# Kernel optimization log

Hardware: AMD Instinct MI355X
Metric: run time of the kernel (lower is better)

## Reference

```python
import jax, jax.numpy as jnp
import numpy as np
import math

D_MODEL = 1024
N_HEADS = 16
D_K = D_MODEL // N_HEADS
B, S = 4, 2048


def setup_inputs() -> dict:
    key = jax.random.key(0)
    ks = jax.random.split(key, 11)
    std = 1.0 / math.sqrt(D_MODEL)
    inp = {
        "query": jax.random.normal(ks[0], (B, S, D_MODEL), dtype=jnp.float32),
        "key_in": jax.random.normal(ks[1], (B, S, D_MODEL), dtype=jnp.float32),
        "value": jax.random.normal(ks[2], (B, S, D_MODEL), dtype=jnp.float32),
        "Wq": jax.random.normal(ks[3], (D_MODEL, D_MODEL), dtype=jnp.float32) * std,
        "bq": jnp.zeros((D_MODEL,), dtype=jnp.float32),
        "Wk": jax.random.normal(ks[4], (D_MODEL, D_MODEL), dtype=jnp.float32) * std,
        "bk": jnp.zeros((D_MODEL,), dtype=jnp.float32),
        "Wv": jax.random.normal(ks[5], (D_MODEL, D_MODEL), dtype=jnp.float32) * std,
        "bv": jnp.zeros((D_MODEL,), dtype=jnp.float32),
        "Wo": jax.random.normal(ks[6], (D_MODEL, D_MODEL), dtype=jnp.float32) * std,
        "bo": jnp.zeros((D_MODEL,), dtype=jnp.float32),
    }
    return inp


def reference(query, key_in, value, Wq, bq, Wk, bk, Wv, bv, Wo, bo):
    b, s, _ = query.shape
    scale = math.sqrt(D_K)
    # projections: nn.Linear computes x @ W.T + b
    Q = (query @ Wq.T + bq).reshape(b, s, N_HEADS, D_K).transpose(0, 2, 1, 3)
    K = (key_in @ Wk.T + bk).reshape(b, s, N_HEADS, D_K).transpose(0, 2, 1, 3)
    V = (value @ Wv.T + bv).reshape(b, s, N_HEADS, D_K).transpose(0, 2, 1, 3)
    # [b, h, s, s]
    scores = jnp.einsum("bhqd,bhkd->bhqk", Q, K) / scale
    causal = jnp.tril(jnp.ones((s, s), dtype=bool))
    scores = jnp.where(causal[None, None, :, :], scores, jnp.float32(-1e9))
    attn = jax.nn.softmax(scores, axis=-1)
    out = jnp.einsum("bhqk,bhkd->bhqd", attn, V)
    out = out.transpose(0, 2, 1, 3).reshape(b, s, D_MODEL)
    return out @ Wo.T + bo
```

## Files before the change

kernel.cpp:

```cpp
#include <hip/hip_runtime.h>
#include <hip/hip_bf16.h>
#include <cstdint>

#define DM   1024
#define NH   16
#define DKK  64
#define BB   4
#define SS   2048

typedef __attribute__((ext_vector_type(8)))  short short8;
typedef __attribute__((ext_vector_type(4)))  float f32x4;
typedef __attribute__((ext_vector_type(16))) float f32x16;

__device__ __forceinline__ unsigned short f2bf(float f) {
    union { float f; uint32_t u; } v; v.f = f;
    uint32_t u = v.u;
    uint32_t r = (u + 0x7FFFu + ((u >> 16) & 1u)) >> 16;
    return (unsigned short)r;
}

__global__ void cvt_all(const float4* __restrict__ q, const float4* __restrict__ k,
                        const float4* __restrict__ v, const float4* __restrict__ wq,
                        const float4* __restrict__ wk, const float4* __restrict__ wv,
                        const float4* __restrict__ wo, ushort4* __restrict__ dst)
{
    const int NA = 2097152, NW = 262144;
    int i = blockIdx.x * 256 + threadIdx.x;
    const float4* s;
    if (i < 3 * NA) {
        int a = i >> 21, off = i & (NA - 1);
        s = (a == 0 ? q : a == 1 ? k : v) + off;
    } else {
        int j = i - 3 * NA;
        int a = j >> 18, off = j & (NW - 1);
        s = (a == 0 ? wq : a == 1 ? wk : a == 2 ? wv : wo) + off;
    }
    float4 f = *s;
    ushort4 o;
    o.x = f2bf(f.x); o.y = f2bf(f.y); o.z = f2bf(f.z); o.w = f2bf(f.w);
    dst[i] = o;
}

__global__ void gemm_qkv(const unsigned short* __restrict__ Aq,
                         const unsigned short* __restrict__ Ak,
                         const unsigned short* __restrict__ Av,
                         const unsigned short* __restrict__ Wq,
                         const unsigned short* __restrict__ Wk,
                         const unsigned short* __restrict__ Wv,
                         const float* __restrict__ bq,
                         const float* __restrict__ bk,
                         const float* __restrict__ bv,
                         unsigned short* __restrict__ Qo,
                         unsigned short* __restrict__ Ko,
                         unsigned short* __restrict__ Vo,
                         const float qscale)
{
    const int z = blockIdx.z;
    const unsigned short* A  = (z == 0) ? Aq : (z == 1) ? Ak : Av;
    const unsigned short* Bw = (z == 0) ? Wq : (z == 1) ? Wk : Wv;
    const float* bias        = (z == 0) ? bq : (z == 1) ? bk : bv;

    __shared__ unsigned short lA[128 * 64];
    __shared__ unsigned short lB[128 * 64];
    const int tid = threadIdx.x;
    const int w = tid >> 6, l = tid & 63;
    const int brow = blockIdx.y * 128;
    const int bcol = blockIdx.x * 128;
    const int wr = (w >> 1) * 64, wc = (w & 1) * 64;
    const int lrow = l & 15;
    const int lk = (l >> 4) * 8;
    const int sr = l >> 3;
    const int sc = (l & 7) * 8;
    f32x4 acc[4][4] = {};

    for (int k0 = 0; k0 < 1024; k0 += 64) {
#pragma unroll
        for (int i = 0; i < 4; ++i) {
            const int chunk = w * 4 + i;
            const int r = chunk * 8 + sr;
            const unsigned short* ga = A  + (size_t)(brow + r) * 1024 + k0 + sc;
            const unsigned short* gb = Bw + (size_t)(bcol + r) * 1024 + k0 + sc;
            __builtin_amdgcn_global_load_lds((__attribute__((address_space(1))) void*)ga,
                                             (__attribute__((address_space(3))) void*)(lA + chunk * 512),
                                             16, 0, 0);
            __builtin_amdgcn_global_load_lds((__attribute__((address_space(1))) void*)gb,
                                             (__attribute__((address_space(3))) void*)(lB + chunk * 512),
                                             16, 0, 0);
        }
        asm volatile("s_waitcnt vmcnt(0)" ::: "memory");
        __syncthreads();
#pragma unroll
        for (int kk = 0; kk < 2; ++kk) {
            short8 af[4], bfr[4];
#pragma unroll
            for (int m = 0; m < 4; ++m)
                af[m] = *(const short8*)(lA + (wr + m * 16 + lrow) * 64 + kk * 32 + lk);
#pragma unroll
            for (int n = 0; n < 4; ++n)
                bfr[n] = *(const short8*)(lB + (wc + n * 16 + lrow) * 64 + kk * 32 + lk);
#pragma unroll
            for (int m = 0; m < 4; ++m)
#pragma unroll
                for (int n = 0; n < 4; ++n)
                    acc[m][n] = __builtin_amdgcn_mfma_f32_16x16x32_bf16(af[m], bfr[n], acc[m][n], 0, 0, 0);
        }
        __syncthreads();
    }

    const float ascale = (z == 0) ? qscale : 1.0f;
#pragma unroll
    for (int m = 0; m < 4; ++m) {
#pragma unroll
        for (int n = 0; n < 4; ++n) {
            const int i0 = brow + wr + m * 16 + (l >> 4) * 4;
            const int j  = bcol + wc + n * 16 + lrow;
            const float bj = bias[j];
            const int hh = j >> 6, d = j & 63;
            if (z < 2) {
                unsigned short* Cb = (z == 0) ? Qo : Ko;
#pragma unroll
                for (int t = 0; t < 4; ++t) {
                    const int i = i0 + t;
                    const int b = i >> 11, s = i & 2047;
                    Cb[(((size_t)(b * NH + hh) * SS) + s) * DKK + d] = f2bf((acc[m][n][t] + bj) * ascale);
                }
            } else {
                const int b = i0 >> 11, s0 = i0 & 2047;
                ushort4 pk;
                pk.x = f2bf(acc[m][n][0] + bj);
                pk.y = f2bf(acc[m][n][1] + bj);
                pk.z = f2bf(acc[m][n][2] + bj);
                pk.w = f2bf(acc[m][n][3] + bj);
                *(ushort4*)(Vo + (((size_t)(b * NH + hh) * DKK) + d) * SS + s0) = pk;
            }
        }
    }
}

__global__ void gemm_out(const unsigned short* __restrict__ A,
                         const unsigned short* __restrict__ Bw,
                         const float* __restrict__ bias,
                         float* __restrict__ Cout)
{
    __shared__ unsigned short lA[128 * 64];
    __shared__ unsigned short lB[128 * 64];
    const int tid = threadIdx.x;
    const int w = tid >> 6, l = tid & 63;
    const int brow = blockIdx.y * 128;
    const int bcol = blockIdx.x * 128;
    const int wr = (w >> 1) * 64, wc = (w & 1) * 64;
    const int lrow = l & 15;
    const int lk = (l >> 4) * 8;
    const int sr = l >> 3;
    const int sc = (l & 7) * 8;
    f32x4 acc[4][4] = {};

    for (int k0 = 0; k0 < 1024; k0 += 64) {
#pragma unroll
        for (int i = 0; i < 4; ++i) {
            const int chunk = w * 4 + i;
            const int r = chunk * 8 + sr;
            const unsigned short* ga = A  + (size_t)(brow + r) * 1024 + k0 + sc;
            const unsigned short* gb = Bw + (size_t)(bcol + r) * 1024 + k0 + sc;
            __builtin_amdgcn_global_load_lds((__attribute__((address_space(1))) void*)ga,
                                             (__attribute__((address_space(3))) void*)(lA + chunk * 512),
                                             16, 0, 0);
            __builtin_amdgcn_global_load_lds((__attribute__((address_space(1))) void*)gb,
                                             (__attribute__((address_space(3))) void*)(lB + chunk * 512),
                                             16, 0, 0);
        }
        asm volatile("s_waitcnt vmcnt(0)" ::: "memory");
        __syncthreads();
#pragma unroll
        for (int kk = 0; kk < 2; ++kk) {
            short8 af[4], bfr[4];
#pragma unroll
            for (int m = 0; m < 4; ++m)
                af[m] = *(const short8*)(lA + (wr + m * 16 + lrow) * 64 + kk * 32 + lk);
#pragma unroll
            for (int n = 0; n < 4; ++n)
                bfr[n] = *(const short8*)(lB + (wc + n * 16 + lrow) * 64 + kk * 32 + lk);
#pragma unroll
            for (int m = 0; m < 4; ++m)
#pragma unroll
                for (int n = 0; n < 4; ++n)
                    acc[m][n] = __builtin_amdgcn_mfma_f32_16x16x32_bf16(af[m], bfr[n], acc[m][n], 0, 0, 0);
        }
        __syncthreads();
    }

#pragma unroll
    for (int m = 0; m < 4; ++m) {
#pragma unroll
        for (int n = 0; n < 4; ++n) {
            const int i0 = brow + wr + m * 16 + (l >> 4) * 4;
            const int j  = bcol + wc + n * 16 + lrow;
            const float bj = bias[j];
#pragma unroll
            for (int t = 0; t < 4; ++t)
                Cout[(size_t)(i0 + t) * DM + j] = acc[m][n][t] + bj;
        }
    }
}

__global__ __launch_bounds__(256) void attn_kernel(
        const unsigned short* __restrict__ Q,
        const unsigned short* __restrict__ K,
        const unsigned short* __restrict__ Vt,
        unsigned short* __restrict__ AO)
{
    const int flat = blockIdx.y * 16 + blockIdx.x;
    const int r8 = flat & 7, k8 = flat >> 3;
    const int bh = r8 * 8 + (k8 & 7);
    const int qchunk = 15 - (k8 >> 3);
    const int tid = threadIdx.x;
    const int w = tid >> 6, l = tid & 63;
    const int ln = l & 31, h = l >> 5;
    const int qb = qchunk * 128;
    const int q0w = qb + w * 32;

    __shared__ __align__(16) char lK[2][4096];
    __shared__ __align__(16) char lV[2][4096];

    const unsigned short* Qp = Q  + ((size_t)bh * SS + q0w) * DKK;
    const unsigned short* Kp = K  + (size_t)bh * SS * DKK;
    const unsigned short* Vp = Vt + (size_t)bh * DKK * SS;

    const int srow = tid >> 3, scb = tid & 7;
    const int swb = srow * 128 + ((scb * 16) ^ ((srow & 7) << 4));
    const unsigned short* ksrc = Kp + srow * DKK + scb * 8;
    const int vd = (scb < 4) ? srow : (srow + 32);
    const unsigned short* vsrc = Vp + (size_t)vd * SS + (scb & 3) * 8;

    int ka[4], va[4];
#pragma unroll
    for (int ks = 0; ks < 4; ++ks)
        ka[ks] = ln * 128 + ((ks * 32 + h * 16) ^ ((ln & 7) << 4));
#pragma unroll
    for (int c = 0; c < 4; ++c)
        va[c] = ln * 128 + ((c * 32 + h * 16) ^ ((ln & 7) << 4));

    short8 qf[4];
#pragma unroll
    for (int ks = 0; ks < 4; ++ks)
        qf[ks] = *(const short8*)(Qp + (size_t)ln * DKK + ks * 16 + h * 8);

    f32x16 o0 = {}, o1 = {};
    float lsum = 0.f;

    const int Tc = qb / 32;
    const int NT = Tc + 4;

    auto compute = [&](int t, int buf) {
        const char* kb = lK[buf];
        const char* vb = lV[buf];
        short8 kf[4];
#pragma unroll
        for (int ks = 0; ks < 4; ++ks) kf[ks] = *(const short8*)(kb + ka[ks]);

        f32x16 s = {};
        __builtin_amdgcn_s_setprio(1);
#pragma unroll
        for (int ks = 0; ks < 4; ++ks)
            s = __builtin_amdgcn_mfma_f32_32x32x16_bf16(kf[ks], qf[ks], s, 0, 0, 0);
        __builtin_amdgcn_s_setprio(0);

        const bool diag = (t == Tc + w);
#pragma unroll
        for (int r = 0; r < 16; ++r) {
            float e;
            asm("v_exp_f32 %0, %1" : "=v"(e) : "v"(s[r]));
            if (diag) {
                const int crow = (r & 3) + 8 * (r >> 2) + 4 * h;
                e = (crow > ln) ? 0.f : e;
            }
            s[r] = e;
            lsum += e;
        }

        uint32_t pk[8];
#pragma unroll
        for (int i = 0; i < 8; ++i) {
            uint32_t d;
            asm("v_cvt_pk_bf16_f32 %0, %1, %2" : "=v"(d) : "v"(s[2 * i]), "v"(s[2 * i + 1]));
            pk[i] = d;
        }
        asm("v_permlane32_swap_b32 %0, %1" : "+v"(pk[0]), "+v"(pk[2]));
        asm("v_permlane32_swap_b32 %0, %1" : "+v"(pk[1]), "+v"(pk[3]));
        asm("v_permlane32_swap_b32 %0, %1" : "+v"(pk[4]), "+v"(pk[6]));
        asm("v_permlane32_swap_b32 %0, %1" : "+v"(pk[5]), "+v"(pk[7]));

        union Ux { uint32_t u[4]; short8 s8; } pa0, pa1;
        pa0.u[0] = pk[0]; pa0.u[1] = pk[1]; pa0.u[2] = pk[2]; pa0.u[3] = pk[3];
        pa1.u[0] = pk[4]; pa1.u[1] = pk[5]; pa1.u[2] = pk[6]; pa1.u[3] = pk[7];

        short8 vf00 = *(const short8*)(vb + va[0]);
        short8 vf10 = *(const short8*)(vb + va[1]);
        short8 vf01 = *(const short8*)(vb + va[2]);
        short8 vf11 = *(const short8*)(vb + va[3]);

        __builtin_amdgcn_s_setprio(1);
        o0 = __builtin_amdgcn_mfma_f32_32x32x16_bf16(pa0.s8, vf00, o0, 0, 0, 0);
        o0 = __builtin_amdgcn_mfma_f32_32x32x16_bf16(pa1.s8, vf10, o0, 0, 0, 0);
        o1 = __builtin_amdgcn_mfma_f32_32x32x16_bf16(pa0.s8, vf01, o1, 0, 0, 0);
        o1 = __builtin_amdgcn_mfma_f32_32x32x16_bf16(pa1.s8, vf11, o1, 0, 0, 0);
        __builtin_amdgcn_s_setprio(0);
    };

    short8 kA = *(const short8*)(ksrc);
    short8 vA = *(const short8*)(vsrc);
    *(short8*)(&lK[0][swb]) = kA;
    *(short8*)(&lV[0][swb]) = vA;
    kA = *(const short8*)(ksrc + 2048);
    vA = *(const short8*)(vsrc + 32);
    short8 kB = {}, vB = {};
    __syncthreads();

    int t = 0, buf = 0;
    for (;;) {
        if (t + 2 < NT) {
            kB = *(const short8*)(ksrc + (size_t)(t + 2) * 2048);
            vB = *(const short8*)(vsrc + (size_t)(t + 2) * 32);
        }
        if (t <= Tc + w) compute(t, buf);
        if (t + 1 < NT) {
            *(short8*)(&lK[buf ^ 1][swb]) = kA;
            *(short8*)(&lV[buf ^ 1][swb]) = vA;
        }
        __syncthreads();
        buf ^= 1;
        if (++t == NT) break;

        if (t + 2 < NT) {
            kA = *(const short8*)(ksrc + (size_t)(t + 2) * 2048);
            vA = *(const short8*)(vsrc + (size_t)(t + 2) * 32);
        }
        if (t <= Tc + w) compute(t, buf);
        if (t + 1 < NT) {
            *(short8*)(&lK[buf ^ 1][swb]) = kB;
            *(short8*)(&lV[buf ^ 1][swb]) = vB;
        }
        __syncthreads();
        buf ^= 1;
        if (++t == NT) break;
    }

    lsum += __shfl_xor(lsum, 32, 64);
    const float rcp = 1.0f / lsum;

    const int bb = bh >> 4, hh = bh & 15;
#pragma unroll
    for (int r = 0; r < 16; ++r) {
        const int crow = (r & 3) + 8 * (r >> 2) + 4 * h;
        const float rl = __shfl(rcp, crow, 64);
        const size_t row = (size_t)(bb * SS + q0w + crow) * DM + hh * DKK;
        AO[row + ln]      = f2bf(o0[r] * rl);
        AO[row + 32 + ln] = f2bf(o1[r] * rl);
    }
}

extern "C" void kernel_launch(void* const* d_in, const int* in_sizes, int n_in,
                              void* d_out, int out_size, void* d_ws, size_t ws_size,
                              hipStream_t stream)
{
    const float* query  = (const float*)d_in[0];
    const float* key_in = (const float*)d_in[1];
    const float* value  = (const float*)d_in[2];
    const float* Wq = (const float*)d_in[3];
    const float* bq = (const float*)d_in[4];
    const float* Wk = (const float*)d_in[5];
    const float* bk = (const float*)d_in[6];
    const float* Wv = (const float*)d_in[7];
    const float* bv = (const float*)d_in[8];
    const float* Wo = (const float*)d_in[9];
    const float* bo = (const float*)d_in[10];

    const size_t NACT = (size_t)BB * SS * DM;
    const size_t NWT  = (size_t)DM * DM;

    unsigned short* ws  = (unsigned short*)d_ws;
    unsigned short* qin = ws;
    unsigned short* kin = qin + NACT;
    unsigned short* vin = kin + NACT;
    unsigned short* wqb = vin + NACT;
    unsigned short* wkb = wqb + NWT;
    unsigned short* wvb = wkb + NWT;
    unsigned short* wob = wvb + NWT;
    unsigned short* Qb  = wob + NWT;
    unsigned short* Kb  = Qb + NACT;
    unsigned short* Vtb = Kb + NACT;
    unsigned short* AOb = Vtb + NACT;

    const int n4 = (int)(3 * (NACT / 4) + 4 * (NWT / 4));
    cvt_all<<<n4 / 256, 256, 0, stream>>>((const float4*)query, (const float4*)key_in,
                                          (const float4*)value, (const float4*)Wq,
                                          (const float4*)Wk, (const float4*)Wv,
                                          (const float4*)Wo, (ushort4*)ws);

    const float QSCALE = 0.125f * 1.44269504088896f;
    dim3 gq(DM / 128, (BB * SS) / 128, 3);
    gemm_qkv<<<gq, 256, 0, stream>>>(qin, kin, vin, wqb, wkb, wvb,
                                     bq, bk, bv, Qb, Kb, Vtb, QSCALE);

    attn_kernel<<<dim3(16, 64), 256, 0, stream>>>(Qb, Kb, Vtb, AOb);

    dim3 gg(DM / 128, (BB * SS) / 128);
    gemm_out<<<gg, 256, 0, stream>>>(AOb, wob, bo, (float*)d_out);
}
```

Baseline: 190.3 us.

## Fuse activation fp32->bf16 conversion into QKV GEMM and remap block order

Removes the separate conversion pass over the three fp32 activation tensors. The QKV GEMM now loads fp32 directly, converts to bf16 in registers with v_cvt_pk_bf16_f32, and writes the result to LDS, so the bf16 copies are never written out and read back. Only the weights are still pre-converted. Both GEMMs also remap block IDs so that consecutive blocks spread across the 8 column tiles, which is meant to improve L2 or per-die cache locality. The cost is that the A-tile loads become synchronous register loads instead of async global_load_lds, and they read twice as many bytes per tile.

Measured after the change: 175.2 us. -7.9%, faster.

```diff
diff --git a/kernel.cpp b/kernel.cpp
--- a/kernel.cpp
+++ b/kernel.cpp
@@ -19,31 +19,23 @@
     return (unsigned short)r;
 }
 
-__global__ void cvt_all(const float4* __restrict__ q, const float4* __restrict__ k,
-                        const float4* __restrict__ v, const float4* __restrict__ wq,
-                        const float4* __restrict__ wk, const float4* __restrict__ wv,
-                        const float4* __restrict__ wo, ushort4* __restrict__ dst)
+__global__ void cvt_w(const float4* __restrict__ wq, const float4* __restrict__ wk,
+                      const float4* __restrict__ wv, const float4* __restrict__ wo,
+                      ushort4* __restrict__ dst)
 {
-    const int NA = 2097152, NW = 262144;
+    const int NW = 262144;
     int i = blockIdx.x * 256 + threadIdx.x;
-    const float4* s;
-    if (i < 3 * NA) {
-        int a = i >> 21, off = i & (NA - 1);
-        s = (a == 0 ? q : a == 1 ? k : v) + off;
-    } else {
-        int j = i - 3 * NA;
-        int a = j >> 18, off = j & (NW - 1);
-        s = (a == 0 ? wq : a == 1 ? wk : a == 2 ? wv : wo) + off;
-    }
+    int a = i >> 18, off = i & (NW - 1);
+    const float4* s = (a == 0 ? wq : a == 1 ? wk : a == 2 ? wv : wo) + off;
     float4 f = *s;
     ushort4 o;
     o.x = f2bf(f.x); o.y = f2bf(f.y); o.z = f2bf(f.z); o.w = f2bf(f.w);
     dst[i] = o;
 }
 
-__global__ void gemm_qkv(const unsigned short* __restrict__ Aq,
-                         const unsigned short* __restrict__ Ak,
-                         const unsigned short* __restrict__ Av,
+__global__ void gemm_qkv(const float* __restrict__ Aq,
+                         const float* __restrict__ Ak,
+                         const float* __restrict__ Av,
                          const unsigned short* __restrict__ Wq,
                          const unsigned short* __restrict__ Wk,
                          const unsigned short* __restrict__ Wv,
@@ -55,8 +47,14 @@
                          unsigned short* __restrict__ Vo,
                          const float qscale)
 {
-    const int z = blockIdx.z;
-    const unsigned short* A  = (z == 0) ? Aq : (z == 1) ? Ak : Av;
+    const int orig = blockIdx.z * 512 + blockIdx.y * 8 + blockIdx.x;
+    const int wid  = (orig & 7) * 192 + (orig >> 3);
+    const int z    = wid >> 9;
+    const int rem  = wid & 511;
+    const int brow = (rem >> 3) * 128;
+    const int bcol = (rem & 7) * 128;
+
+    const float* A           = (z == 0) ? Aq : (z == 1) ? Ak : Av;
     const unsigned short* Bw = (z == 0) ? Wq : (z == 1) ? Wk : Wv;
     const float* bias        = (z == 0) ? bq : (z == 1) ? bk : bv;
 
@@ -64,8 +62,6 @@
     __shared__ unsigned short lB[128 * 64];
     const int tid = threadIdx.x;
     const int w = tid >> 6, l = tid & 63;
-    const int brow = blockIdx.y * 128;
-    const int bcol = blockIdx.x * 128;
     const int wr = (w >> 1) * 64, wc = (w & 1) * 64;
     const int lrow = l & 15;
     const int lk = (l >> 4) * 8;
@@ -78,14 +74,24 @@
         for (int i = 0; i < 4; ++i) {
             const int chunk = w * 4 + i;
             const int r = chunk * 8 + sr;
-            const unsigned short* ga = A  + (size_t)(brow + r) * 1024 + k0 + sc;
             const unsigned short* gb = Bw + (size_t)(bcol + r) * 1024 + k0 + sc;
-            __builtin_amdgcn_global_load_lds((__attribute__((address_space(1))) void*)ga,
-                                             (__attribute__((address_space(3))) void*)(lA + chunk * 512),
-                                             16, 0, 0);
             __builtin_amdgcn_global_load_lds((__attribute__((address_space(1))) void*)gb,
                                              (__attribute__((address_space(3))) void*)(lB + chunk * 512),
                                              16, 0, 0);
+        }
+#pragma unroll
+        for (int i = 0; i < 4; ++i) {
+            const int chunk = w * 4 + i;
+            const int r = chunk * 8 + sr;
+            const float* ga = A + (size_t)(brow + r) * 1024 + k0 + sc;
+            float4 f0 = *(const float4*)(ga);
+            float4 f1 = *(const float4*)(ga + 4);
+            union { uint32_t u[4]; short8 s8; } c;
+            asm("v_cvt_pk_bf16_f32 %0, %1, %2" : "=v"(c.u[0]) : "v"(f0.x), "v"(f0.y));
+            asm("v_cvt_pk_bf16_f32 %0, %1, %2" : "=v"(c.u[1]) : "v"(f0.z), "v"(f0.w));
+            asm("v_cvt_pk_bf16_f32 %0, %1, %2" : "=v"(c.u[2]) : "v"(f1.x), "v"(f1.y));
+            asm("v_cvt_pk_bf16_f32 %0, %1, %2" : "=v"(c.u[3]) : "v"(f1.z), "v"(f1.w));
+            *(short8*)((char*)lA + chunk * 1024 + sr * 128 + sc * 2) = c.s8;
         }
         asm volatile("s_waitcnt vmcnt(0)" ::: "memory");
         __syncthreads();
@@ -142,12 +148,15 @@
                          const float* __restrict__ bias,
                          float* __restrict__ Cout)
 {
+    const int orig = blockIdx.y * 8 + blockIdx.x;
+    const int wid  = (orig & 7) * 64 + (orig >> 3);
+    const int brow = (wid >> 3) * 128;
+    const int bcol = (wid & 7) * 128;
+
     __shared__ unsigned short lA[128 * 64];
     __shared__ unsigned short lB[128 * 64];
     const int tid = threadIdx.x;
     const int w = tid >> 6, l = tid & 63;
-    const int brow = blockIdx.y * 128;
-    const int bcol = blockIdx.x * 128;
     const int wr = (w >> 1) * 64, wc = (w & 1) * 64;
     const int lrow = l & 15;
     const int lk = (l >> 4) * 8;
@@ -379,10 +388,7 @@
     const size_t NWT  = (size_t)DM * DM;
 
     unsigned short* ws  = (unsigned short*)d_ws;
-    unsigned short* qin = ws;
-    unsigned short* kin = qin + NACT;
-    unsigned short* vin = kin + NACT;
-    unsigned short* wqb = vin + NACT;
+    unsigned short* wqb = ws;
     unsigned short* wkb = wqb + NWT;
     unsigned short* wvb = wkb + NWT;
     unsigned short* wob = wvb + NWT;
@@ -391,15 +397,14 @@
     unsigned short* Vtb = Kb + NACT;
     unsigned short* AOb = Vtb + NACT;
 
-    const int n4 = (int)(3 * (NACT / 4) + 4 * (NWT / 4));
-    cvt_all<<<n4 / 256, 256, 0, stream>>>((const float4*)query, (const float4*)key_in,
-                                          (const float4*)value, (const float4*)Wq,
-                                          (const float4*)Wk, (const float4*)Wv,
-                                          (const float4*)Wo, (ushort4*)ws);
+    const int n4 = (int)(4 * (NWT / 4));
+    cvt_w<<<n4 / 256, 256, 0, stream>>>((const float4*)Wq, (const float4*)Wk,
+                                        (const float4*)Wv, (const float4*)Wo,
+                                        (ushort4*)ws);
 
     const float QSCALE = 0.125f * 1.44269504088896f;
     dim3 gq(DM / 128, (BB * SS) / 128, 3);
-    gemm_qkv<<<gq, 256, 0, stream>>>(qin, kin, vin, wqb, wkb, wvb,
+    gemm_qkv<<<gq, 256, 0, stream>>>(query, key_in, value, wqb, wkb, wvb,
                                      bq, bk, bv, Qb, Kb, Vtb, QSCALE);
 
     attn_kernel<<<dim3(16, 64), 256, 0, stream>>>(Qb, Kb, Vtb, AOb);
```
